# Performance work log

Hardware: AMD Instinct MI355X
Metric: run time of the kernel (lower is better)

The kernel has to match this reference:

```python
import jax, jax.numpy as jnp
import numpy as np


def _layernorm(x, w, b, eps=1e-5):
    mu = x.mean(-1, keepdims=True)
    var = ((x - mu) ** 2).mean(-1, keepdims=True)
    return (x - mu) / jnp.sqrt(var + eps) * w + b


def _conv_res3d(x, w, b):
    # Conv3d(k=3, pad=1) + InstanceNorm3d (no affine) + LeakyReLU(0.01), residual add
    y = jax.lax.conv_general_dilated(x, w, (1, 1, 1), 'SAME',
                                     dimension_numbers=('NCDHW', 'OIDHW', 'NCDHW'))
    y = y + b[None, :, None, None, None]
    mu = y.mean((2, 3, 4), keepdims=True)
    var = ((y - mu) ** 2).mean((2, 3, 4), keepdims=True)
    y = (y - mu) / jnp.sqrt(var + 1e-5)
    y = jnp.where(y >= 0, y, 0.01 * y)
    return x + y


def _ssm(xl, delta_w, delta_b, Bp_w, Cp_w, A_log):
    # xl: [n, l, d_inner]; selective scan with lax.scan over l
    A = -jax.nn.softplus(A_log)                                   # [d_state], broadcast over d_inner
    delta = jnp.clip(jax.nn.softplus(xl @ delta_w.T + delta_b), 1e-4, 10.0)
    Bm = xl @ Bp_w.T                                              # [n, l, d_state]
    Cm = xl @ Cp_w.T
    n, l, di = xl.shape
    ds = A_log.shape[0]

    def step(h, inp):
        d_t, x_t, b_t, c_t = inp                                  # [n,di],[n,di],[n,ds],[n,ds]
        A_bar = jnp.exp(d_t[:, :, None] * A)                      # [n,di,ds]
        h = A_bar * h + (d_t * x_t)[:, :, None] * b_t[:, None, :]
        y = jnp.einsum('nds,ns->nd', h, c_t)
        return h, y

    h0 = jnp.zeros((n, di, ds), xl.dtype)
    _, ys = jax.lax.scan(step, h0, (jnp.swapaxes(delta, 0, 1), jnp.swapaxes(xl, 0, 1),
                                    jnp.swapaxes(Bm, 0, 1), jnp.swapaxes(Cm, 0, 1)))
    return jnp.swapaxes(ys, 0, 1)                                 # [n, l, d_inner]


def _mamba(x, p):
    # x: [n, l, d_model] (already layer-normed)
    left = x @ p['left_w'].T                                      # [n, l, d_inner]
    left = jnp.swapaxes(left, 1, 2)                               # [n, d_inner, l]
    dc = p['conv1d_w'].shape[-1]
    left = jnp.pad(left, ((0, 0), (0, 0), (dc - 1, 0)))           # causal pad
    left = jax.lax.conv_general_dilated(left, p['conv1d_w'], (1,), 'VALID',
                                        feature_group_count=p['conv1d_w'].shape[0],
                                        dimension_numbers=('NCH', 'OIH', 'NCH'))
    left = left + p['conv1d_b'][None, :, None]
    left = jax.nn.silu(jnp.swapaxes(left, 1, 2))                  # [n, l, d_inner]
    y = _ssm(left, p['delta_w'], p['delta_b'], p['Bp_w'], p['Cp_w'], p['A_log'])
    gate = jax.nn.silu(x @ p['right_w'].T)
    out = _layernorm(y * gate, p['pn_w'], p['pn_b'])
    return out @ p['out_w'].T                                     # [n, l, d_model]


def reference(x, cr1_w, cr1_b, cr2_w, cr2_b, ln_w, ln_b, left_w, conv1d_w, conv1d_b,
              delta_w, delta_b, Bp_w, Cp_w, A_log, right_w, pn_w, pn_b, out_w,
              res_scale, axis_w):
    p = dict(left_w=left_w, conv1d_w=conv1d_w, conv1d_b=conv1d_b, delta_w=delta_w,
             delta_b=delta_b, Bp_w=Bp_w, Cp_w=Cp_w, A_log=A_log, right_w=right_w,
             pn_w=pn_w, pn_b=pn_b, out_w=out_w)
    identity = x
    B, C, H, W, D = x.shape
    x = _conv_res3d(x, cr1_w, cr1_b)
    x = _conv_res3d(x, cr2_w, cr2_b)

    xh = jnp.transpose(x, (0, 3, 4, 2, 1)).reshape(B * W * D, H, C)
    mh = _mamba(_layernorm(xh, ln_w, ln_b), p).reshape(B, W, D, H, C).transpose(0, 4, 3, 1, 2)

    xw = jnp.transpose(x, (0, 2, 4, 3, 1)).reshape(B * H * D, W, C)
    mw = _mamba(_layernorm(xw, ln_w, ln_b), p).reshape(B, H, D, W, C).transpose(0, 4, 1, 3, 2)

    xd = jnp.transpose(x, (0, 2, 3, 4, 1)).reshape(B * H * W, D, C)
    md = _mamba(_layernorm(xd, ln_w, ln_b), p).reshape(B, H, W, D, C).transpose(0, 4, 1, 2, 3)

    w = jax.nn.softmax(axis_w)
    out = w[0] * mh + w[1] * mw + w[2] * md
    return identity + res_scale * out


def setup_inputs() -> dict:
    key = jax.random.key(0)
    ks = jax.random.split(key, 12)
    B, C, H, W, D = 2, 64, 32, 32, 32
    ds, dc = 16, 4
    di = 2 * C
    f32 = jnp.float32

    def xav(k, shape):
        fan_in, fan_out = shape[-1], shape[0]
        return jax.random.normal(k, shape, f32) * np.sqrt(2.0 / (fan_in + fan_out))

    return {
        'x': jax.random.normal(ks[0], (B, C, H, W, D), f32),
        'cr1_w': jax.random.normal(ks[1], (C, C, 3, 3, 3), f32) / np.sqrt(C * 27),
        'cr1_b': jnp.zeros((C,), f32),
        'cr2_w': jax.random.normal(ks[2], (C, C, 3, 3, 3), f32) / np.sqrt(C * 27),
        'cr2_b': jnp.zeros((C,), f32),
        'ln_w': jnp.ones((C,), f32),
        'ln_b': jnp.zeros((C,), f32),
        'left_w': xav(ks[3], (di, C)),
        'conv1d_w': jax.random.normal(ks[4], (di, 1, dc), f32) / np.sqrt(dc),
        'conv1d_b': jnp.zeros((di,), f32),
        'delta_w': jax.random.normal(ks[5], (di, di), f32) / np.sqrt(di),
        'delta_b': jnp.zeros((di,), f32),
        'Bp_w': jax.random.normal(ks[6], (ds, di), f32) / np.sqrt(di),
        'Cp_w': jax.random.normal(ks[7], (ds, di), f32) / np.sqrt(di),
        'A_log': jnp.log(jnp.arange(1, ds + 1, dtype=f32)),
        'right_w': xav(ks[8], (di, C)),
        'pn_w': jnp.ones((di,), f32),
        'pn_b': jnp.zeros((di,), f32),
        'out_w': xav(ks[9], (C, di)),
        'res_scale': jnp.asarray(0.1, f32),
        'axis_w': jnp.zeros((3,), f32),
    }
```

## Files before the change

### kernel.cpp

```cpp
#include <hip/hip_runtime.h>
#include <hip/hip_bf16.h>
#include <math.h>
#include <stdint.h>


typedef __attribute__((ext_vector_type(8))) short short8;
typedef __attribute__((ext_vector_type(4))) float f32x4;

__device__ __forceinline__ float siluf(float x){ return x * (1.0f / (1.0f + __expf(-x))); }
__device__ __forceinline__ float softplusf(float x){ return fmaxf(x, 0.0f) + log1pf(__expf(-fabsf(x))); }
__device__ __forceinline__ float softplus_hw(float x){
  float t = __builtin_amdgcn_exp2f(-fabsf(x) * 1.44269504088896f);
  return fmaxf(x, 0.0f) + 0.69314718055995f * __builtin_amdgcn_logf(1.0f + t);
}
__device__ __forceinline__ float b2f(short s){
  unsigned int u = ((unsigned int)(unsigned short)s) << 16;
  float f; __builtin_memcpy(&f, &u, 4); return f;
}
__device__ __forceinline__ short f2b(float v){
  __hip_bfloat16 h = __float2bfloat16(v);
  unsigned short u; __builtin_memcpy(&u, &h, 2); return (short)u;
}

__device__ __forceinline__ void gld_lds16(const void* g, void* l){
  __builtin_amdgcn_global_load_lds(
      (__attribute__((address_space(1))) void*)(uintptr_t)g,
      (__attribute__((address_space(3))) void*)(uint32_t)(uintptr_t)l,
      16, 0, 0);
}

__global__ __launch_bounds__(256) void setup_k(uint4* __restrict__ xz,
    const float* __restrict__ cr1w, const float* __restrict__ cr2w,
    const float* __restrict__ lw, const float* __restrict__ rwt,
    const float* __restrict__ dwt, const float* __restrict__ bw,
    const float* __restrict__ cwp, const float* __restrict__ owt,
    const float* __restrict__ alog,
    __hip_bfloat16* __restrict__ W4a, __hip_bfloat16* __restrict__ W4b,
    __hip_bfloat16* __restrict__ Wlr, __hip_bfloat16* __restrict__ Wd,
    __hip_bfloat16* __restrict__ oWp, float* __restrict__ negA2,
    uint4* __restrict__ statz)
{
  int i = blockIdx.x * 256 + threadIdx.x;
  if (i < 628864){ uint4 z; z.x = z.y = z.z = z.w = 0u; xz[i] = z; return; }
  i -= 628864;
  if (i < 110592){
    int tap = i >> 12, co = (i >> 6) & 63, ci = i & 63;
    W4a[i] = __float2bfloat16(cr1w[(co * 64 + ci) * 27 + tap]); return;
  }
  i -= 110592;
  if (i < 110592){
    int tap = i >> 12, co = (i >> 6) & 63, ci = i & 63;
    W4b[i] = __float2bfloat16(cr2w[(co * 64 + ci) * 27 + tap]); return;
  }
  i -= 110592;
  if (i < 16384){
    int row = i >> 6, c = i & 63;
    float v = (row < 128) ? lw[row * 64 + c] : rwt[(row - 128) * 64 + c];
    Wlr[i] = __float2bfloat16(v); return;
  }
  i -= 16384;
  if (i < 20480){
    int row = i >> 7, k = i & 127;
    float v = (row < 128) ? dwt[row * 128 + k]
            : (row < 144 ? bw[(row - 128) * 128 + k] : cwp[(row - 144) * 128 + k]);
    Wd[i] = __float2bfloat16(v); return;
  }
  i -= 20480;
  if (i < 8192){ oWp[i] = __float2bfloat16(owt[i]); return; }
  i -= 8192;
  if (i < 16){ negA2[i] = -softplusf(alog[i]) * 1.44269504088896f; return; }
  i -= 16;
  if (i < 128){ uint4 z; z.x = z.y = z.z = z.w = 0u; statz[i] = z; return; }
}

__global__ __launch_bounds__(256) void pack_k(const float* __restrict__ xin,
                                              __hip_bfloat16* __restrict__ xpad)
{
  __shared__ float lds[64 * 33];
  const int t = threadIdx.x, blk = blockIdx.x;
  const int b = blk >> 10, h = (blk >> 5) & 31, w = blk & 31;
  const size_t rbase = ((size_t)(b * 64) << 15) + h * 1024 + w * 32;
  #pragma unroll
  for (int r = 0; r < 8; r++){
    int c = r * 8 + (t >> 5), d = t & 31;
    lds[c * 33 + d] = xin[rbase + (size_t)c * 32768 + d];
  }
  __syncthreads();
  const size_t wbase = (size_t)b * 2515456 + (size_t)(h + 1) * 73984 + (w + 1) * 2176 + 64;
  #pragma unroll
  for (int r = 0; r < 8; r++){
    int d = r * 4 + (t >> 6), c = t & 63;
    xpad[wbase + d * 64 + c] = __float2bfloat16(lds[c * 33 + d]);
  }
}

__global__ __launch_bounds__(256) void conv_mfma_k(const __hip_bfloat16* __restrict__ xpad,
    const __hip_bfloat16* __restrict__ W4, __hip_bfloat16* __restrict__ y,
    float* __restrict__ stats)
{
  __shared__ short smem[12288];

  const int t = threadIdx.x;
  const int wave = t >> 6, lane = t & 63;
  const int quad = lane >> 4, ln = lane & 15;

  const int blk = blockIdx.x;
  const int xcd = blk & 7, j = blk >> 3;
  const int b = j >> 5, jj = j & 31;
  const int h = xcd * 4 + (jj >> 3);
  const int w0 = (jj & 7) * 4;

  const int bcol = (lane >> 2) * 64 + (lane & 3) * 8;
  const __hip_bfloat16* Bg = xpad + (size_t)b * 2515456 + (size_t)h * 73984
                                  + (size_t)(w0 + wave) * 2176 + bcol;
  const __hip_bfloat16* Ag = W4 + wave * 1024 + bcol;
  short* Bl0 = &smem[wave * 2048];
  short* Bl1 = &smem[wave * 2048 + 512];
  short* Bl2 = &smem[wave * 2048 + 1024];
  short* Bl3 = &smem[wave * 2048 + 1536];
  short* Al0 = &smem[8192 + wave * 512];
  short* Al1 = &smem[8192 + 2048 + wave * 512];

  f32x4 acc[2][4];
  #pragma unroll
  for (int jn = 0; jn < 2; jn++)
    #pragma unroll
    for (int m = 0; m < 4; m++) acc[jn][m] = (f32x4){0.f, 0.f, 0.f, 0.f};

  const int aoff = ln * 32 + quad * 8;
  const int boff = wave * 2048 + ln * 32 + quad * 8;

  for (int t1 = 0; t1 < 27; t1++){
    const int ki = t1 / 9, kj = (t1 / 3) % 3, kk = t1 % 3;
    const int tapoff = ki * 73984 + kj * 2176 + kk * 64;

    __syncthreads();
    gld_lds16(Bg + tapoff,             Bl0);
    gld_lds16(Bg + tapoff + 1024,      Bl1);
    gld_lds16(Bg + tapoff + 32,        Bl2);
    gld_lds16(Bg + tapoff + 1024 + 32, Bl3);
    gld_lds16(Ag + t1 * 4096,          Al0);
    gld_lds16(Ag + t1 * 4096 + 32,     Al1);
    __syncthreads();

    {
      short8 a0 = *(const short8*)&smem[8192 + aoff];
      short8 a1 = *(const short8*)&smem[8192 + 512 + aoff];
      short8 a2 = *(const short8*)&smem[8192 + 1024 + aoff];
      short8 a3 = *(const short8*)&smem[8192 + 1536 + aoff];
      short8 b0 = *(const short8*)&smem[boff];
      short8 b1 = *(const short8*)&smem[boff + 512];
      acc[0][0] = __builtin_amdgcn_mfma_f32_16x16x32_bf16(a0, b0, acc[0][0], 0, 0, 0);
      acc[0][1] = __builtin_amdgcn_mfma_f32_16x16x32_bf16(a1, b0, acc[0][1], 0, 0, 0);
      acc[0][2] = __builtin_amdgcn_mfma_f32_16x16x32_bf16(a2, b0, acc[0][2], 0, 0, 0);
      acc[0][3] = __builtin_amdgcn_mfma_f32_16x16x32_bf16(a3, b0, acc[0][3], 0, 0, 0);
      acc[1][0] = __builtin_amdgcn_mfma_f32_16x16x32_bf16(a0, b1, acc[1][0], 0, 0, 0);
      acc[1][1] = __builtin_amdgcn_mfma_f32_16x16x32_bf16(a1, b1, acc[1][1], 0, 0, 0);
      acc[1][2] = __builtin_amdgcn_mfma_f32_16x16x32_bf16(a2, b1, acc[1][2], 0, 0, 0);
      acc[1][3] = __builtin_amdgcn_mfma_f32_16x16x32_bf16(a3, b1, acc[1][3], 0, 0, 0);
    }
    {
      short8 a0 = *(const short8*)&smem[8192 + 2048 + aoff];
      short8 a1 = *(const short8*)&smem[8192 + 2048 + 512 + aoff];
      short8 a2 = *(const short8*)&smem[8192 + 2048 + 1024 + aoff];
      short8 a3 = *(const short8*)&smem[8192 + 2048 + 1536 + aoff];
      short8 b0 = *(const short8*)&smem[boff + 1024];
      short8 b1 = *(const short8*)&smem[boff + 1536];
      acc[0][0] = __builtin_amdgcn_mfma_f32_16x16x32_bf16(a0, b0, acc[0][0], 0, 0, 0);
      acc[0][1] = __builtin_amdgcn_mfma_f32_16x16x32_bf16(a1, b0, acc[0][1], 0, 0, 0);
      acc[0][2] = __builtin_amdgcn_mfma_f32_16x16x32_bf16(a2, b0, acc[0][2], 0, 0, 0);
      acc[0][3] = __builtin_amdgcn_mfma_f32_16x16x32_bf16(a3, b0, acc[0][3], 0, 0, 0);
      acc[1][0] = __builtin_amdgcn_mfma_f32_16x16x32_bf16(a0, b1, acc[1][0], 0, 0, 0);
      acc[1][1] = __builtin_amdgcn_mfma_f32_16x16x32_bf16(a1, b1, acc[1][1], 0, 0, 0);
      acc[1][2] = __builtin_amdgcn_mfma_f32_16x16x32_bf16(a2, b1, acc[1][2], 0, 0, 0);
      acc[1][3] = __builtin_amdgcn_mfma_f32_16x16x32_bf16(a3, b1, acc[1][3], 0, 0, 0);
    }
  }

  const size_t sbase = (size_t)h * 1024 + (w0 + wave) * 32 + ln;
  #pragma unroll
  for (int jn = 0; jn < 2; jn++){
    #pragma unroll
    for (int mt = 0; mt < 4; mt++){
      #pragma unroll
      for (int reg = 0; reg < 4; reg++){
        int co = mt * 16 + quad * 4 + reg;
        y[(((size_t)(b * 64 + co)) << 15) + sbase + jn * 16] = __float2bfloat16(acc[jn][mt][reg]);
      }
    }
  }

  __syncthreads();
  float* sred = (float*)smem;
  #pragma unroll
  for (int mt = 0; mt < 4; mt++){
    #pragma unroll
    for (int reg = 0; reg < 4; reg++){
      float a0 = acc[0][mt][reg], a1 = acc[1][mt][reg];
      float s = a0 + a1, s2 = a0 * a0 + a1 * a1;
      #pragma unroll
      for (int m = 1; m < 16; m <<= 1){
        s  += __shfl_xor(s, m);
        s2 += __shfl_xor(s2, m);
      }
      if (ln == 0){
        const int idx = (((wave * 4 + quad) * 4 + mt) * 4 + reg) * 2;
        sred[idx] = s; sred[idx + 1] = s2;
      }
    }
  }
  __syncthreads();
  if (t < 128){
    const int k = t & 1, reg = (t >> 1) & 3, mt = (t >> 3) & 3, q = t >> 5;
    float v = 0.f;
    #pragma unroll
    for (int wv = 0; wv < 4; wv++)
      v += sred[(((wv * 4 + q) * 4 + mt) * 4 + reg) * 2 + k];
    const int co = mt * 16 + q * 4 + reg;
    atomicAdd(&stats[k * 128 + b * 64 + co], v);
  }
}

__global__ __launch_bounds__(256) void apply_pack_k(const float* __restrict__ xin,
    const __hip_bfloat16* __restrict__ y, const float* __restrict__ stats,
    __hip_bfloat16* __restrict__ x1b, __hip_bfloat16* __restrict__ xpad)
{
  __shared__ float lds[64 * 33];
  const int t = threadIdx.x, blk = blockIdx.x;
  const int b = blk >> 10, h = (blk >> 5) & 31, w = blk & 31;
  const size_t rbase = ((size_t)(b * 64) << 15) + h * 1024 + w * 32;
  const int c = t >> 2, d0 = (t & 3) * 8;
  const float s1v = stats[b * 64 + c], s2v = stats[128 + b * 64 + c];
  const float mu = s1v * (1.0f / 32768.0f);
  const float var = s2v * (1.0f / 32768.0f) - mu * mu;
  const float rs = rsqrtf(fmaxf(var, 0.f) + 1e-5f);
  const size_t idx = rbase + (size_t)c * 32768 + d0;
  short8 yv = *(const short8*)&y[idx];
  float4 xa = *(const float4*)&xin[idx];
  float4 xb = *(const float4*)&xin[idx + 4];
  short8 o;
  #pragma unroll
  for (int jj = 0; jj < 8; jj++){
    float v = (b2f(yv[jj]) - mu) * rs;
    v = (v >= 0.0f) ? v : 0.01f * v;
    v += (jj < 4) ? ((const float*)&xa)[jj] : ((const float*)&xb)[jj - 4];
    o[jj] = f2b(v);
    lds[c * 33 + d0 + jj] = v;
  }
  *(short8*)&x1b[idx] = o;
  __syncthreads();
  const size_t wbase = (size_t)b * 2515456 + (size_t)(h + 1) * 73984 + (w + 1) * 2176 + 64;
  #pragma unroll
  for (int r = 0; r < 8; r++){
    int d = r * 4 + (t >> 6), cc = t & 63;
    xpad[wbase + d * 64 + cc] = __float2bfloat16(lds[cc * 33 + d]);
  }
}

__global__ __launch_bounds__(256) void apply_ln_k(const __hip_bfloat16* __restrict__ x1b,
    const __hip_bfloat16* __restrict__ y, const float* __restrict__ stats,
    const float* __restrict__ lnw, const float* __restrict__ lnb,
    __hip_bfloat16* __restrict__ lnx)
{
  __shared__ float lds[64 * 33];
  __shared__ float s_mu[32], s_rs[32];
  const int t = threadIdx.x, blk = blockIdx.x;
  const int b = blk >> 10, h = (blk >> 5) & 31, w = blk & 31;
  const size_t rbase = ((size_t)(b * 64) << 15) + h * 1024 + w * 32;
  const int c = t >> 2, d0 = (t & 3) * 8;
  const float s1v = stats[b * 64 + c], s2v = stats[128 + b * 64 + c];
  const float mu0 = s1v * (1.0f / 32768.0f);
  const float var0 = s2v * (1.0f / 32768.0f) - mu0 * mu0;
  const float rs0 = rsqrtf(fmaxf(var0, 0.f) + 1e-5f);
  const size_t idx = rbase + (size_t)c * 32768 + d0;
  short8 yv = *(const short8*)&y[idx];
  short8 xv = *(const short8*)&x1b[idx];
  #pragma unroll
  for (int jj = 0; jj < 8; jj++){
    float v = (b2f(yv[jj]) - mu0) * rs0;
    v = (v >= 0.0f) ? v : 0.01f * v;
    lds[c * 33 + d0 + jj] = v + b2f(xv[jj]);
  }
  __syncthreads();
  if (t < 32){
    float s = 0.f, s2 = 0.f;
    for (int cc = 0; cc < 64; cc++){ float v = lds[cc * 33 + t]; s += v; s2 += v * v; }
    float mu = s * (1.f / 64.f);
    float var = s2 * (1.f / 64.f) - mu * mu;
    s_mu[t] = mu; s_rs[t] = rsqrtf(var + 1e-5f);
  }
  __syncthreads();
  const int d = t >> 3, c0 = (t & 7) * 8;
  const int pos = b * 32768 + h * 1024 + w * 32 + d;
  const float mu = s_mu[d], rs = s_rs[d];
  short8 o;
  #pragma unroll
  for (int jj = 0; jj < 8; jj++){
    int cc = c0 + jj;
    o[jj] = f2b((lds[cc * 33 + d] - mu) * rs * lnw[cc] + lnb[cc]);
  }
  *(short8*)&lnx[(size_t)pos * 64 + c0] = o;
}

__global__ __launch_bounds__(256) void gemm_lr_k(const __hip_bfloat16* __restrict__ lnx,
    const __hip_bfloat16* __restrict__ Wlr, __hip_bfloat16* __restrict__ Lb,
    __hip_bfloat16* __restrict__ Gb)
{
  const int t = threadIdx.x, wave = t >> 6, lane = t & 63, quad = lane >> 4, ln = lane & 15;
  const int pos0 = blockIdx.x * 64 + wave * 16;
  f32x4 acc[16];
  #pragma unroll
  for (int nt = 0; nt < 16; nt++) acc[nt] = (f32x4){0.f, 0.f, 0.f, 0.f};
  #pragma unroll
  for (int ks = 0; ks < 2; ks++){
    short8 a = *(const short8*)&lnx[(size_t)(pos0 + ln) * 64 + ks * 32 + quad * 8];
    #pragma unroll
    for (int nt = 0; nt < 16; nt++){
      short8 bv = *(const short8*)&Wlr[(nt * 16 + ln) * 64 + ks * 32 + quad * 8];
      acc[nt] = __builtin_amdgcn_mfma_f32_16x16x32_bf16(a, bv, acc[nt], 0, 0, 0);
    }
  }
  #pragma unroll
  for (int nt = 0; nt < 16; nt++){
    int col = nt * 16 + ln;
    #pragma unroll
    for (int reg = 0; reg < 4; reg++){
      int pos = pos0 + quad * 4 + reg;
      float v = acc[nt][reg];
      if (col < 128) Lb[(size_t)pos * 128 + col] = __float2bfloat16(v);
      else           Gb[(size_t)pos * 128 + col - 128] = __float2bfloat16(siluf(v));
    }
  }
}

__global__ __launch_bounds__(256) void dbcscan_k(const __hip_bfloat16* __restrict__ Lb,
    const float* __restrict__ cw, const float* __restrict__ cb,
    const __hip_bfloat16* __restrict__ Wd, const float* __restrict__ db,
    const __hip_bfloat16* __restrict__ Gb, const float* __restrict__ negA2,
    const float* __restrict__ pnw, const float* __restrict__ pnb,
    const float* __restrict__ axw,
    __hip_bfloat16* __restrict__ Y0, __hip_bfloat16* __restrict__ Y1,
    __hip_bfloat16* __restrict__ Y2)
{
  __shared__ short s_xl[64 * 136];
  __shared__ short s_d[64 * 128];
  __shared__ short s_Bh[2][32][16];
  __shared__ short s_Ch[2][32][16];
  __shared__ float s_stat[2][32][2];

  const int t = threadIdx.x;
  const int bid = blockIdx.x;
  const int axis = bid % 3;
  const int j = bid / 3;
  int sigma;
  if (axis == 0)      sigma = 1024;
  else if (axis == 1) sigma = 32;
  else                sigma = 1;
  __hip_bfloat16* Yax = (axis == 0) ? Y0 : (axis == 1) ? Y1 : Y2;

  int bases[2];
  #pragma unroll
  for (int s = 0; s < 2; s++){
    const int seq = j * 2 + s;
    const int b = seq >> 10, r1 = (seq >> 5) & 31, r0 = seq & 31;
    if (axis == 0)      bases[s] = b * 32768 + r1 * 32 + r0;
    else if (axis == 1) bases[s] = b * 32768 + r1 * 1024 + r0;
    else                bases[s] = b * 32768 + r1 * 1024 + r0 * 32;
  }

  {
    const int c0 = (t & 15) * 8;
    const int pibase = t >> 4;
    float4 w4[8]; float cbv[8];
    #pragma unroll
    for (int c = 0; c < 8; c++){ w4[c] = *(const float4*)&cw[(c0 + c) * 4]; cbv[c] = cb[c0 + c]; }
    #pragma unroll
    for (int r = 0; r < 4; r++){
      const int row = pibase + r * 16;
      const int sl_ = row >> 5, l = row & 31;
      const int pos = bases[sl_] + l * sigma;
      float acc[8];
      #pragma unroll
      for (int c = 0; c < 8; c++) acc[c] = cbv[c];
      #pragma unroll
      for (int jt = 0; jt < 4; jt++){
        const int off = 3 - jt;
        if (l >= off){
          short8 lv = *(const short8*)&Lb[(size_t)(pos - off * sigma) * 128 + c0];
          #pragma unroll
          for (int c = 0; c < 8; c++){
            float wv = (jt == 0) ? w4[c].x : (jt == 1) ? w4[c].y : (jt == 2) ? w4[c].z : w4[c].w;
            acc[c] += wv * b2f(lv[c]);
          }
        }
      }
      short8 o;
      #pragma unroll
      for (int c = 0; c < 8; c++) o[c] = f2b(siluf(acc[c]));
      *(short8*)&s_xl[row * 136 + c0] = o;
    }
  }
  __syncthreads();

  const int wave = t >> 6, lane = t & 63, quad = lane >> 4, ln = lane & 15;
  {
    const int rowb = (wave * 16 + ln) * 136;
    f32x4 acc2[10];
    #pragma unroll
    for (int nt = 0; nt < 10; nt++) acc2[nt] = (f32x4){0.f, 0.f, 0.f, 0.f};
    #pragma unroll
    for (int ks = 0; ks < 4; ks++){
      short8 a = *(const short8*)&s_xl[rowb + ks * 32 + quad * 8];
      #pragma unroll
      for (int nt = 0; nt < 10; nt++){
        short8 bv = *(const short8*)&Wd[(nt * 16 + ln) * 128 + ks * 32 + quad * 8];
        acc2[nt] = __builtin_amdgcn_mfma_f32_16x16x32_bf16(a, bv, acc2[nt], 0, 0, 0);
      }
    }
    const int row0 = wave * 16 + quad * 4;
    #pragma unroll
    for (int nt = 0; nt < 10; nt++){
      const int col = nt * 16 + ln;
      const bool isd = col < 128;
      const float dbv = isd ? db[col] : 0.f;
      #pragma unroll
      for (int reg = 0; reg < 4; reg++){
        const int row = row0 + reg;
        float v = acc2[nt][reg];
        if (isd){
          v = fminf(fmaxf(softplus_hw(v + dbv), 1e-4f), 10.f);
          s_d[row * 128 + col] = f2b(v);
        } else {
          const int sl_ = row >> 5, l = row & 31, cc = col - 128;
          if (cc < 16) s_Bh[sl_][l][cc] = f2b(v);
          else         s_Ch[sl_][l][cc - 16] = f2b(v);
        }
      }
    }
  }

  float A2[16], h[16];
  #pragma unroll
  for (int s = 0; s < 16; s++){ A2[s] = negA2[s]; h[s] = 0.f; }
  const int sl = wave >> 1;
  const int half = wave & 1;
  const int ch = half * 64 + lane;
  const int base = bases[sl];
  const size_t sx = (size_t)sigma * 128;
  const __hip_bfloat16* pg = Gb + (size_t)base * 128 + ch;

  __syncthreads();

  unsigned short gu = *(const unsigned short*)pg;
  #pragma unroll
  for (int l = 0; l < 32; l++){
    unsigned short ngu = 0;
    if (l + 1 < 32) ngu = *(const unsigned short*)(pg + sx);
    const int row = sl * 32 + l;
    float dt = b2f(s_d[row * 128 + ch]);
    float xt = b2f(s_xl[row * 136 + ch]);
    float g = b2f((short)gu);
    float dx = dt * xt;
    short8 Bv0 = *(const short8*)&s_Bh[sl][l][0];
    short8 Bv1 = *(const short8*)&s_Bh[sl][l][8];
    short8 Cv0 = *(const short8*)&s_Ch[sl][l][0];
    short8 Cv1 = *(const short8*)&s_Ch[sl][l][8];
    float y = 0.f;
    #pragma unroll
    for (int s = 0; s < 16; s++){
      const float Bf = b2f((s < 8) ? Bv0[s] : Bv1[s - 8]);
      const float Cf = b2f((s < 8) ? Cv0[s] : Cv1[s - 8]);
      h[s] = __builtin_amdgcn_exp2f(dt * A2[s]) * h[s] + dx * Bf;
      y += h[s] * Cf;
    }
    s_d[row * 128 + ch] = f2b(y * g);
    gu = ngu;
    pg += sx;
  }
  __syncthreads();

  {
    const int row = t >> 2, part = t & 3;
    const int sl2 = row >> 5, l2 = row & 31;
    const short* yr = &s_d[row * 128 + part * 32];
    float s1 = 0.f, s2 = 0.f;
    #pragma unroll
    for (int i = 0; i < 32; i++){
      float v = b2f(yr[i]);
      s1 += v; s2 += v * v;
    }
    s1 += __shfl_xor(s1, 1); s2 += __shfl_xor(s2, 1);
    s1 += __shfl_xor(s1, 2); s2 += __shfl_xor(s2, 2);
    if (part == 0){ s_stat[sl2][l2][0] = s1; s_stat[sl2][l2][1] = s2; }
  }
  __syncthreads();

  float a0 = axw[0], a1 = axw[1], a2 = axw[2];
  float mxw = fmaxf(a0, fmaxf(a1, a2));
  float e0 = __expf(a0 - mxw), e1 = __expf(a1 - mxw), e2 = __expf(a2 - mxw);
  float wax = ((axis == 0) ? e0 : (axis == 1) ? e1 : e2) / (e0 + e1 + e2);
  const float pw = pnw[ch], pb = pnb[ch];

  __hip_bfloat16* py = Yax + (size_t)base * 128 + ch;
  #pragma unroll
  for (int l = 0; l < 32; l++){
    float ss1 = s_stat[sl][l][0];
    float ss2 = s_stat[sl][l][1];
    float mu = ss1 * (1.f / 128.f);
    float var = ss2 * (1.f / 128.f) - mu * mu;
    float rs = rsqrtf(fmaxf(var, 0.f) + 1e-5f);
    float yv = b2f(s_d[(sl * 32 + l) * 128 + ch]);
    float o = ((yv - mu) * rs * pw + pb) * wax;
    *(unsigned short*)py = (unsigned short)f2b(o);
    py += sx;
  }
}

__global__ __launch_bounds__(256) void gemm_out_k(const __hip_bfloat16* __restrict__ Y0,
    const __hip_bfloat16* __restrict__ Y1, const __hip_bfloat16* __restrict__ Y2,
    const __hip_bfloat16* __restrict__ oW, const float* __restrict__ xres,
    const float* __restrict__ rsc, float* __restrict__ outp)
{
  const int t = threadIdx.x, wave = t >> 6, lane = t & 63, quad = lane >> 4, ln = lane & 15;
  const int pos0 = blockIdx.x * 64 + wave * 16;
  f32x4 acc[4];
  #pragma unroll
  for (int mt = 0; mt < 4; mt++) acc[mt] = (f32x4){0.f, 0.f, 0.f, 0.f};
  #pragma unroll
  for (int ks = 0; ks < 4; ks++){
    const size_t boffs = (size_t)(pos0 + ln) * 128 + ks * 32 + quad * 8;
    short8 bv0 = *(const short8*)&Y0[boffs];
    short8 bv1 = *(const short8*)&Y1[boffs];
    short8 bv2 = *(const short8*)&Y2[boffs];
    #pragma unroll
    for (int mt = 0; mt < 4; mt++){
      short8 a = *(const short8*)&oW[(mt * 16 + ln) * 128 + ks * 32 + quad * 8];
      acc[mt] = __builtin_amdgcn_mfma_f32_16x16x32_bf16(a, bv0, acc[mt], 0, 0, 0);
      acc[mt] = __builtin_amdgcn_mfma_f32_16x16x32_bf16(a, bv1, acc[mt], 0, 0, 0);
      acc[mt] = __builtin_amdgcn_mfma_f32_16x16x32_bf16(a, bv2, acc[mt], 0, 0, 0);
    }
  }
  float rs = rsc[0];
  const int pos = pos0 + ln;
  const int bb = pos >> 15, hwd = pos & 32767;
  #pragma unroll
  for (int mt = 0; mt < 4; mt++){
    #pragma unroll
    for (int reg = 0; reg < 4; reg++){
      int co = mt * 16 + quad * 4 + reg;
      size_t idx = (((size_t)(bb * 64 + co)) << 15) + hwd;
      outp[idx] = xres[idx] + rs * acc[mt][reg];
    }
  }
}

extern "C" void kernel_launch(void* const* d_in, const int* in_sizes, int n_in,
                              void* d_out, int out_size, void* d_ws, size_t ws_size,
                              hipStream_t stream)
{
  const float* x      = (const float*)d_in[0];
  const float* cr1w   = (const float*)d_in[1];
  const float* cr2w   = (const float*)d_in[3];
  const float* ln_w   = (const float*)d_in[5];
  const float* ln_b   = (const float*)d_in[6];
  const float* left_w = (const float*)d_in[7];
  const float* c1dw   = (const float*)d_in[8];
  const float* c1db   = (const float*)d_in[9];
  const float* dw     = (const float*)d_in[10];
  const float* db     = (const float*)d_in[11];
  const float* bpw    = (const float*)d_in[12];
  const float* cpw    = (const float*)d_in[13];
  const float* alog   = (const float*)d_in[14];
  const float* rw     = (const float*)d_in[15];
  const float* pnw    = (const float*)d_in[16];
  const float* pnb    = (const float*)d_in[17];
  const float* ow     = (const float*)d_in[18];
  const float* rsc    = (const float*)d_in[19];
  const float* axw    = (const float*)d_in[20];
  float* out = (float*)d_out;
  float* wsf = (float*)d_ws;

  __hip_bfloat16* ybuf = (__hip_bfloat16*)d_out;
  __hip_bfloat16* x1b  = (__hip_bfloat16*)wsf;
  float* stats1 = wsf + 4194304;
  float* stats2 = wsf + 4194560;
  float* negA2  = wsf + 4194816;
  __hip_bfloat16* W4a  = (__hip_bfloat16*)(wsf + 4195072);
  __hip_bfloat16* W4b  = W4a + 110592;
  __hip_bfloat16* Wlr  = (__hip_bfloat16*)(wsf + 4305664);
  __hip_bfloat16* Wdbc = (__hip_bfloat16*)(wsf + 4313856);
  __hip_bfloat16* oWp  = (__hip_bfloat16*)(wsf + 4324096);
  __hip_bfloat16* xpad = (__hip_bfloat16*)(wsf + 4328192);
  __hip_bfloat16* lnx  = xpad;
  __hip_bfloat16* Lbuf = (__hip_bfloat16*)(wsf + 6843648);
  __hip_bfloat16* Gbuf = (__hip_bfloat16*)(wsf + 11037952);
  __hip_bfloat16* Y0   = (__hip_bfloat16*)wsf;
  __hip_bfloat16* Y1   = (__hip_bfloat16*)(wsf + 15232256);
  __hip_bfloat16* Y2   = (__hip_bfloat16*)(wsf + 19426560);

  setup_k<<<3498, 256, 0, stream>>>((uint4*)xpad, cr1w, cr2w, left_w, rw, dw, bpw, cpw, ow,
                                    alog, W4a, W4b, Wlr, Wdbc, oWp, negA2,
                                    (uint4*)stats1);

  pack_k<<<2048, 256, 0, stream>>>(x, xpad);
  conv_mfma_k<<<512, 256, 0, stream>>>(xpad, W4a, ybuf, stats1);
  apply_pack_k<<<2048, 256, 0, stream>>>(x, ybuf, stats1, x1b, xpad);
  conv_mfma_k<<<512, 256, 0, stream>>>(xpad, W4b, ybuf, stats2);
  apply_ln_k<<<2048, 256, 0, stream>>>(x1b, ybuf, stats2, ln_w, ln_b, lnx);

  gemm_lr_k<<<1024, 256, 0, stream>>>(lnx, Wlr, Lbuf, Gbuf);

  dbcscan_k<<<3072, 256, 0, stream>>>(Lbuf, c1dw, c1db, Wdbc, db, Gbuf, negA2,
                                      pnw, pnb, axw, Y0, Y1, Y2);

  gemm_out_k<<<1024, 256, 0, stream>>>(Y0, Y1, Y2, oWp, x, rsc, out);
}
```

Baseline: 409.9 us.

## Double-buffer conv tap loads and fuse layernorm into left/right GEMM

The 3D conv kernel now double-buffers its LDS tiles, prefetching the next tap's input and weight slices while MFMAs run on the current buffer. This removes one barrier per tap and overlaps global-to-LDS copies with compute, at the cost of twice the shared memory per block. Separately, the apply-instance-norm/layernorm kernel is fused with the left/right projection GEMM. The normalized tile stays in LDS instead of round-tripping through global memory, which also removes one launch.

Measured after the change: 394.0 us. 1.04x faster.

```diff
diff --git a/kernel.cpp b/kernel.cpp
--- a/kernel.cpp
+++ b/kernel.cpp
@@ -98,7 +98,7 @@
     const __hip_bfloat16* __restrict__ W4, __hip_bfloat16* __restrict__ y,
     float* __restrict__ stats)
 {
-  __shared__ short smem[12288];
+  __shared__ short smem[24576];
 
   const int t = threadIdx.x;
   const int wave = t >> 6, lane = t & 63;
@@ -114,12 +114,6 @@
   const __hip_bfloat16* Bg = xpad + (size_t)b * 2515456 + (size_t)h * 73984
                                   + (size_t)(w0 + wave) * 2176 + bcol;
   const __hip_bfloat16* Ag = W4 + wave * 1024 + bcol;
-  short* Bl0 = &smem[wave * 2048];
-  short* Bl1 = &smem[wave * 2048 + 512];
-  short* Bl2 = &smem[wave * 2048 + 1024];
-  short* Bl3 = &smem[wave * 2048 + 1536];
-  short* Al0 = &smem[8192 + wave * 512];
-  short* Al1 = &smem[8192 + 2048 + wave * 512];
 
   f32x4 acc[2][4];
   #pragma unroll
@@ -128,28 +122,40 @@
     for (int m = 0; m < 4; m++) acc[jn][m] = (f32x4){0.f, 0.f, 0.f, 0.f};
 
   const int aoff = ln * 32 + quad * 8;
-  const int boff = wave * 2048 + ln * 32 + quad * 8;
-
+  const int boffl = wave * 2048 + ln * 32 + quad * 8;
+
+  {
+    short* S = &smem[0];
+    gld_lds16(Bg,              S + wave * 2048);
+    gld_lds16(Bg + 1024,       S + wave * 2048 + 512);
+    gld_lds16(Bg + 32,         S + wave * 2048 + 1024);
+    gld_lds16(Bg + 1024 + 32,  S + wave * 2048 + 1536);
+    gld_lds16(Ag,              S + 8192 + wave * 512);
+    gld_lds16(Ag + 32,         S + 8192 + 2048 + wave * 512);
+  }
+  int cur = 0;
   for (int t1 = 0; t1 < 27; t1++){
-    const int ki = t1 / 9, kj = (t1 / 3) % 3, kk = t1 % 3;
-    const int tapoff = ki * 73984 + kj * 2176 + kk * 64;
-
     __syncthreads();
-    gld_lds16(Bg + tapoff,             Bl0);
-    gld_lds16(Bg + tapoff + 1024,      Bl1);
-    gld_lds16(Bg + tapoff + 32,        Bl2);
-    gld_lds16(Bg + tapoff + 1024 + 32, Bl3);
-    gld_lds16(Ag + t1 * 4096,          Al0);
-    gld_lds16(Ag + t1 * 4096 + 32,     Al1);
-    __syncthreads();
-
+    if (t1 + 1 < 27){
+      const int t2 = t1 + 1;
+      const int ki = t2 / 9, kj = (t2 / 3) % 3, kk = t2 % 3;
+      const int tapoff = ki * 73984 + kj * 2176 + kk * 64;
+      short* S = &smem[(cur ^ 1) * 12288];
+      gld_lds16(Bg + tapoff,             S + wave * 2048);
+      gld_lds16(Bg + tapoff + 1024,      S + wave * 2048 + 512);
+      gld_lds16(Bg + tapoff + 32,        S + wave * 2048 + 1024);
+      gld_lds16(Bg + tapoff + 1024 + 32, S + wave * 2048 + 1536);
+      gld_lds16(Ag + t2 * 4096,          S + 8192 + wave * 512);
+      gld_lds16(Ag + t2 * 4096 + 32,     S + 8192 + 2048 + wave * 512);
+    }
+    const int sb = cur * 12288;
     {
-      short8 a0 = *(const short8*)&smem[8192 + aoff];
-      short8 a1 = *(const short8*)&smem[8192 + 512 + aoff];
-      short8 a2 = *(const short8*)&smem[8192 + 1024 + aoff];
-      short8 a3 = *(const short8*)&smem[8192 + 1536 + aoff];
-      short8 b0 = *(const short8*)&smem[boff];
-      short8 b1 = *(const short8*)&smem[boff + 512];
+      short8 a0 = *(const short8*)&smem[sb + 8192 + aoff];
+      short8 a1 = *(const short8*)&smem[sb + 8192 + 512 + aoff];
+      short8 a2 = *(const short8*)&smem[sb + 8192 + 1024 + aoff];
+      short8 a3 = *(const short8*)&smem[sb + 8192 + 1536 + aoff];
+      short8 b0 = *(const short8*)&smem[sb + boffl];
+      short8 b1 = *(const short8*)&smem[sb + boffl + 512];
       acc[0][0] = __builtin_amdgcn_mfma_f32_16x16x32_bf16(a0, b0, acc[0][0], 0, 0, 0);
       acc[0][1] = __builtin_amdgcn_mfma_f32_16x16x32_bf16(a1, b0, acc[0][1], 0, 0, 0);
       acc[0][2] = __builtin_amdgcn_mfma_f32_16x16x32_bf16(a2, b0, acc[0][2], 0, 0, 0);
@@ -160,12 +166,12 @@
       acc[1][3] = __builtin_amdgcn_mfma_f32_16x16x32_bf16(a3, b1, acc[1][3], 0, 0, 0);
     }
     {
-      short8 a0 = *(const short8*)&smem[8192 + 2048 + aoff];
-      short8 a1 = *(const short8*)&smem[8192 + 2048 + 512 + aoff];
-      short8 a2 = *(const short8*)&smem[8192 + 2048 + 1024 + aoff];
-      short8 a3 = *(const short8*)&smem[8192 + 2048 + 1536 + aoff];
-      short8 b0 = *(const short8*)&smem[boff + 1024];
-      short8 b1 = *(const short8*)&smem[boff + 1536];
+      short8 a0 = *(const short8*)&smem[sb + 8192 + 2048 + aoff];
+      short8 a1 = *(const short8*)&smem[sb + 8192 + 2048 + 512 + aoff];
+      short8 a2 = *(const short8*)&smem[sb + 8192 + 2048 + 1024 + aoff];
+      short8 a3 = *(const short8*)&smem[sb + 8192 + 2048 + 1536 + aoff];
+      short8 b0 = *(const short8*)&smem[sb + boffl + 1024];
+      short8 b1 = *(const short8*)&smem[sb + boffl + 1536];
       acc[0][0] = __builtin_amdgcn_mfma_f32_16x16x32_bf16(a0, b0, acc[0][0], 0, 0, 0);
       acc[0][1] = __builtin_amdgcn_mfma_f32_16x16x32_bf16(a1, b0, acc[0][1], 0, 0, 0);
       acc[0][2] = __builtin_amdgcn_mfma_f32_16x16x32_bf16(a2, b0, acc[0][2], 0, 0, 0);
@@ -175,6 +181,7 @@
       acc[1][2] = __builtin_amdgcn_mfma_f32_16x16x32_bf16(a2, b1, acc[1][2], 0, 0, 0);
       acc[1][3] = __builtin_amdgcn_mfma_f32_16x16x32_bf16(a3, b1, acc[1][3], 0, 0, 0);
     }
+    cur ^= 1;
   }
 
   const size_t sbase = (size_t)h * 1024 + (w0 + wave) * 32 + ln;
@@ -257,63 +264,74 @@
   }
 }
 
-__global__ __launch_bounds__(256) void apply_ln_k(const __hip_bfloat16* __restrict__ x1b,
+__global__ __launch_bounds__(256) void ln_lr_k(const __hip_bfloat16* __restrict__ x1b,
     const __hip_bfloat16* __restrict__ y, const float* __restrict__ stats,
     const float* __restrict__ lnw, const float* __restrict__ lnb,
-    __hip_bfloat16* __restrict__ lnx)
-{
-  __shared__ float lds[64 * 33];
-  __shared__ float s_mu[32], s_rs[32];
+    const __hip_bfloat16* __restrict__ Wlr, __hip_bfloat16* __restrict__ Lb,
+    __hip_bfloat16* __restrict__ Gb)
+{
+  __shared__ float lds_v[2][64 * 33];
+  __shared__ float s_mu[64], s_rs[64];
+  __shared__ short s_ln[64 * 68];
+
   const int t = threadIdx.x, blk = blockIdx.x;
-  const int b = blk >> 10, h = (blk >> 5) & 31, w = blk & 31;
-  const size_t rbase = ((size_t)(b * 64) << 15) + h * 1024 + w * 32;
+  const int b = blk >> 9;
+  const int h = (blk >> 4) & 31;
+  const int w0 = (blk & 15) * 2;
+
   const int c = t >> 2, d0 = (t & 3) * 8;
   const float s1v = stats[b * 64 + c], s2v = stats[128 + b * 64 + c];
   const float mu0 = s1v * (1.0f / 32768.0f);
   const float var0 = s2v * (1.0f / 32768.0f) - mu0 * mu0;
   const float rs0 = rsqrtf(fmaxf(var0, 0.f) + 1e-5f);
-  const size_t idx = rbase + (size_t)c * 32768 + d0;
-  short8 yv = *(const short8*)&y[idx];
-  short8 xv = *(const short8*)&x1b[idx];
-  #pragma unroll
-  for (int jj = 0; jj < 8; jj++){
-    float v = (b2f(yv[jj]) - mu0) * rs0;
-    v = (v >= 0.0f) ? v : 0.01f * v;
-    lds[c * 33 + d0 + jj] = v + b2f(xv[jj]);
-  }
-  __syncthreads();
-  if (t < 32){
+  #pragma unroll
+  for (int wl = 0; wl < 2; wl++){
+    const size_t rbase = ((size_t)(b * 64) << 15) + h * 1024 + (w0 + wl) * 32;
+    const size_t idx = rbase + (size_t)c * 32768 + d0;
+    short8 yv = *(const short8*)&y[idx];
+    short8 xv = *(const short8*)&x1b[idx];
+    #pragma unroll
+    for (int jj = 0; jj < 8; jj++){
+      float v = (b2f(yv[jj]) - mu0) * rs0;
+      v = (v >= 0.0f) ? v : 0.01f * v;
+      lds_v[wl][c * 33 + d0 + jj] = v + b2f(xv[jj]);
+    }
+  }
+  __syncthreads();
+
+  if (t < 64){
+    const int wl = t >> 5, d = t & 31;
     float s = 0.f, s2 = 0.f;
-    for (int cc = 0; cc < 64; cc++){ float v = lds[cc * 33 + t]; s += v; s2 += v * v; }
+    for (int cc = 0; cc < 64; cc++){
+      float v = lds_v[wl][cc * 33 + d];
+      s += v; s2 += v * v;
+    }
     float mu = s * (1.f / 64.f);
     float var = s2 * (1.f / 64.f) - mu * mu;
     s_mu[t] = mu; s_rs[t] = rsqrtf(var + 1e-5f);
   }
   __syncthreads();
-  const int d = t >> 3, c0 = (t & 7) * 8;
-  const int pos = b * 32768 + h * 1024 + w * 32 + d;
-  const float mu = s_mu[d], rs = s_rs[d];
-  short8 o;
-  #pragma unroll
-  for (int jj = 0; jj < 8; jj++){
-    int cc = c0 + jj;
-    o[jj] = f2b((lds[cc * 33 + d] - mu) * rs * lnw[cc] + lnb[cc]);
-  }
-  *(short8*)&lnx[(size_t)pos * 64 + c0] = o;
-}
-
-__global__ __launch_bounds__(256) void gemm_lr_k(const __hip_bfloat16* __restrict__ lnx,
-    const __hip_bfloat16* __restrict__ Wlr, __hip_bfloat16* __restrict__ Lb,
-    __hip_bfloat16* __restrict__ Gb)
-{
-  const int t = threadIdx.x, wave = t >> 6, lane = t & 63, quad = lane >> 4, ln = lane & 15;
-  const int pos0 = blockIdx.x * 64 + wave * 16;
+
+  {
+    const int pos_loc = t >> 2, c0 = (t & 3) * 16;
+    const int wl = pos_loc >> 5, d = pos_loc & 31;
+    const float mu = s_mu[pos_loc], rs = s_rs[pos_loc];
+    #pragma unroll
+    for (int k = 0; k < 16; k++){
+      const int cc = c0 + k;
+      s_ln[pos_loc * 68 + cc] = f2b((lds_v[wl][cc * 33 + d] - mu) * rs * lnw[cc] + lnb[cc]);
+    }
+  }
+  __syncthreads();
+
+  const int wave = t >> 6, lane = t & 63, quad = lane >> 4, ln = lane & 15;
+  const int pos0 = blk * 64 + wave * 16;
   f32x4 acc[16];
   #pragma unroll
   for (int nt = 0; nt < 16; nt++) acc[nt] = (f32x4){0.f, 0.f, 0.f, 0.f};
   #pragma unroll
   for (int ks = 0; ks < 2; ks++){
-    short8 a = *(const short8*)&lnx[(size_t)(pos0 + ln) * 64 + ks * 32 + quad * 8];
+    short8 a = *(const short8*)&s_ln[(wave * 16 + ln) * 68 + ks * 32 + quad * 8];
     #pragma unroll
     for (int nt = 0; nt < 16; nt++){
       short8 bv = *(const short8*)&Wlr[(nt * 16 + ln) * 64 + ks * 32 + quad * 8];
@@ -591,7 +609,6 @@
   __hip_bfloat16* Wdbc = (__hip_bfloat16*)(wsf + 4313856);
   __hip_bfloat16* oWp  = (__hip_bfloat16*)(wsf + 4324096);
   __hip_bfloat16* xpad = (__hip_bfloat16*)(wsf + 4328192);
-  __hip_bfloat16* lnx  = xpad;
   __hip_bfloat16* Lbuf = (__hip_bfloat16*)(wsf + 6843648);
   __hip_bfloat16* Gbuf = (__hip_bfloat16*)(wsf + 11037952);
   __hip_bfloat16* Y0   = (__hip_bfloat16*)wsf;
@@ -606,9 +623,7 @@
   conv_mfma_k<<<512, 256, 0, stream>>>(xpad, W4a, ybuf, stats1);
   apply_pack_k<<<2048, 256, 0, stream>>>(x, ybuf, stats1, x1b, xpad);
   conv_mfma_k<<<512, 256, 0, stream>>>(xpad, W4b, ybuf, stats2);
-  apply_ln_k<<<2048, 256, 0, stream>>>(x1b, ybuf, stats2, ln_w, ln_b, lnx);
-
-  gemm_lr_k<<<1024, 256, 0, stream>>>(lnx, Wlr, Lbuf, Gbuf);
+  ln_lr_k<<<1024, 256, 0, stream>>>(x1b, ybuf, stats2, ln_w, ln_b, Wlr, Lbuf, Gbuf);
 
   dbcscan_k<<<3072, 256, 0, stream>>>(Lbuf, c1dw, c1db, Wdbc, db, Gbuf, negA2,
                                       pnw, pnb, axw, Y0, Y1, Y2);
```
